# Kernel optimization log

Measured on AMD Instinct MI355X. Metric: run time of the kernel, lower is better.

The kernel has to match this reference:

```python
import jax, jax.numpy as jnp
import numpy as np

ALPHA = 0.2        # LeakyReLU negative slope (config['alpha'])
NEG_INF = -9e15    # mask value from the original code


def setup_inputs() -> dict:
    key = jax.random.key(0)
    k1, k2, k3, k4 = jax.random.split(key, 4)
    N, Fin, Fout = 8192, 512, 256
    inp = jax.random.normal(k1, (N, Fin), dtype=jnp.float32)
    adj = jax.random.randint(k2, (N, N), 0, 2, dtype=jnp.int32)
    # xavier_uniform with gain=1.414
    limW = 1.414 * np.sqrt(6.0 / (Fin + Fout))
    W = jax.random.uniform(k3, (Fin, Fout), dtype=jnp.float32, minval=-limW, maxval=limW)
    lima = 1.414 * np.sqrt(6.0 / (2 * Fout + 1))
    a = jax.random.uniform(k4, (2 * Fout, 1), dtype=jnp.float32, minval=-lima, maxval=lima)
    return {"input": inp, "adj": adj, "W": W, "a": a}


def reference(input, adj, W, a):
    # h: [N, F]
    h = input @ W
    Fout = W.shape[1]
    # The original builds a_input[i, j] = concat(h_i, h_j) and dots with a.
    # Equivalently: e_ij = leakyrelu(h_i . a[:F] + h_j . a[F:]), computed
    # without the O(N^2 * 2F) intermediate.
    s1 = h @ a[:Fout, 0]   # [N] contribution from node i
    s2 = h @ a[Fout:, 0]   # [N] contribution from node j
    e = s1[:, None] + s2[None, :]                     # [N, N]
    e = jnp.where(e > 0, e, ALPHA * e)                # LeakyReLU
    scores = jnp.where(adj > 0, e, NEG_INF)
    attention = jax.nn.softmax(scores, axis=1)        # row-wise softmax
    # dropout is identity in inference mode (training=False)
    h_prime = attention @ h                           # [N, F]
    return jax.nn.elu(h_prime)                        # concat=True path
```

## Files before the change

kernel.cpp:

```cpp
#include <hip/hip_runtime.h>
#include <stdint.h>
#include <stddef.h>


#define N_NODES 8192
#define FIN     512
#define FOUT    256
#define LRALPHA 0.2f
#define MI_SHIFT 16.0f

typedef float f32x4 __attribute__((ext_vector_type(4)));
typedef short s16x8 __attribute__((ext_vector_type(8)));
typedef unsigned short u16x4 __attribute__((ext_vector_type(4)));
typedef int   i32x4 __attribute__((ext_vector_type(4)));

__device__ __forceinline__ short f2bf_rne(float f) {
  uint32_t u = __builtin_bit_cast(uint32_t, f);
  u += 0x7fffu + ((u >> 16) & 1u);
  return (short)(u >> 16);
}
__device__ __forceinline__ short f2bf_fast(float f) {
  uint32_t u = __builtin_bit_cast(uint32_t, f);
  return (short)((u + 0x8000u) >> 16);
}
__device__ __forceinline__ float bf2f(short s) {
  uint32_t u = ((uint32_t)(uint16_t)s) << 16;
  return __builtin_bit_cast(float, u);
}

__global__ __launch_bounds__(256) void k_prep(const float* __restrict__ W,
                                              uint16_t* __restrict__ WThi,
                                              uint16_t* __restrict__ WTlo) {
  const int idx = blockIdx.x * 256 + threadIdx.x;
  const int n = idx >> 9;
  const int k = idx & 511;
  float v = W[k * FOUT + n];
  short h = f2bf_rne(v);
  WThi[idx] = (uint16_t)h;
  WTlo[idx] = (uint16_t)f2bf_rne(v - bf2f(h));
}

__global__ __launch_bounds__(256) void k_gemm_fused(const float* __restrict__ X,
                                                    const uint16_t* __restrict__ WThi,
                                                    const uint16_t* __restrict__ WTlo,
                                                    const float* __restrict__ a,
                                                    uint16_t* __restrict__ HT,
                                                    float* __restrict__ s1g,
                                                    float* __restrict__ s2g) {
  __shared__ float ls1[16], ls2[16];
  __shared__ uint16_t tile[FOUT * 16];
  const int lane = threadIdx.x & 63;
  const int w    = threadIdx.x >> 6;
  const int m    = lane & 15;
  const int quad = lane >> 4;
  const int i0   = blockIdx.x * 16;
  const int colg = w * 64;

  f32x4 acc[4];
#pragma unroll
  for (int cb = 0; cb < 4; ++cb) { f32x4 z = {0.f,0.f,0.f,0.f}; acc[cb] = z; }

  for (int kt = 0; kt < FIN / 32; ++kt) {
    const int k0 = kt * 32 + quad * 8;
    const float* ap = X + (size_t)(i0 + m) * FIN + k0;
    f32x4 a0 = *(const f32x4*)ap;
    f32x4 a1 = *(const f32x4*)(ap + 4);
    s16x8 ahi, alo;
#pragma unroll
    for (int e = 0; e < 4; ++e) {
      short h0 = f2bf_rne(a0[e]); ahi[e] = h0; alo[e] = f2bf_rne(a0[e] - bf2f(h0));
      short h1 = f2bf_rne(a1[e]); ahi[4+e] = h1; alo[4+e] = f2bf_rne(a1[e] - bf2f(h1));
    }
#pragma unroll
    for (int cb = 0; cb < 4; ++cb) {
      const int n = colg + cb * 16 + m;
      s16x8 bhi = *(const s16x8*)(WThi + (size_t)n * FIN + k0);
      s16x8 blo = *(const s16x8*)(WTlo + (size_t)n * FIN + k0);
      acc[cb] = __builtin_amdgcn_mfma_f32_16x16x32_bf16(ahi, bhi, acc[cb], 0, 0, 0);
      acc[cb] = __builtin_amdgcn_mfma_f32_16x16x32_bf16(ahi, blo, acc[cb], 0, 0, 0);
      acc[cb] = __builtin_amdgcn_mfma_f32_16x16x32_bf16(alo, bhi, acc[cb], 0, 0, 0);
    }
  }

  float p1[4] = {0.f,0.f,0.f,0.f}, p2[4] = {0.f,0.f,0.f,0.f};
#pragma unroll
  for (int cb = 0; cb < 4; ++cb) {
    const int n = colg + cb * 16 + m;
    const float a1c = a[n];
    const float a2c = a[FOUT + n];
#pragma unroll
    for (int reg = 0; reg < 4; ++reg) {
      p1[reg] += acc[cb][reg] * a1c;
      p2[reg] += acc[cb][reg] * a2c;
    }
  }
#pragma unroll
  for (int off = 1; off <= 8; off <<= 1)
#pragma unroll
    for (int reg = 0; reg < 4; ++reg) {
      p1[reg] += __shfl_xor(p1[reg], off);
      p2[reg] += __shfl_xor(p2[reg], off);
    }
  if (threadIdx.x < 16) { ls1[threadIdx.x] = 0.f; ls2[threadIdx.x] = 0.f; }
  __syncthreads();
  if (m == 0) {
#pragma unroll
    for (int reg = 0; reg < 4; ++reg) {
      atomicAdd(&ls1[quad * 4 + reg], p1[reg]);
      atomicAdd(&ls2[quad * 4 + reg], p2[reg]);
    }
  }
#pragma unroll
  for (int cb = 0; cb < 4; ++cb) {
    const int col = colg + cb * 16 + m;
    u16x4 pk;
#pragma unroll
    for (int reg = 0; reg < 4; ++reg) pk[reg] = (uint16_t)f2bf_rne(acc[cb][reg]);
    *(u16x4*)(tile + col * 16 + quad * 4) = pk;
  }
  __syncthreads();
  const int t = threadIdx.x;
  if (t < 16) { s1g[i0 + t] = ls1[t]; s2g[i0 + t] = ls2[t]; }
  const uint4* src = (const uint4*)(tile + t * 16);
  uint4 v0 = src[0], v1 = src[1];
  uint4* dst = (uint4*)(HT + (size_t)t * N_NODES + i0);
  dst[0] = v0; dst[1] = v1;
}

__global__ __launch_bounds__(512, 4) void k_attn(const int* __restrict__ adj,
                                                 const uint16_t* __restrict__ HT,
                                                 const float* __restrict__ s1,
                                                 const float* __restrict__ s2,
                                                 float* __restrict__ pout,
                                                 float* __restrict__ pden,
                                                 int split) {
  extern __shared__ char smem[];
  uint16_t* Pl     = (uint16_t*)smem;
  float*    ldsden = (float*)(smem + 16384);
  float*    ls2    = (float*)(smem + 17408);

  const int tid  = threadIdx.x;
  const int lane = tid & 63;
  const int w    = tid >> 6;
  const int m    = lane & 15;
  const int q    = lane >> 4;
  const int i0   = blockIdx.x * 32;
  const int sp   = blockIdx.y;
  const int jrange = N_NODES / split;
  const int jbeg   = sp * jrange;
  const int nphase = jrange / 128;
  const int colg = w * 32;
  const int rtp  = q >> 1;
  const int jq   = (q & 1) * 8;
  const int prow = i0 + rtp * 16 + m;

  for (int o = tid * 4; o < jrange; o += 2048)
    *(f32x4*)(ls2 + o) = *(const f32x4*)(s2 + jbeg + o);

  const float s1r = s1[prow];
  float mi = s1r + MI_SHIFT; mi = mi > 0.f ? mi : LRALPHA * mi;

  f32x4 acc[2][2];
#pragma unroll
  for (int rt = 0; rt < 2; ++rt)
#pragma unroll
    for (int cb = 0; cb < 2; ++cb) { f32x4 z = {0.f,0.f,0.f,0.f}; acc[rt][cb] = z; }
  float den = 0.f;

  const int* arow = adj + (size_t)prow * N_NODES + jbeg + w * 16 + jq;
  const int  pwoff = ((w * 2 + (q & 1)) * 32 + rtp * 16 + m) * 8;

  i32x4 A0 = *(const i32x4*)arow;
  i32x4 A1 = *(const i32x4*)(arow + 4);
  __syncthreads();

#pragma unroll 1
  for (int p = 0; p < nphase; ++p) {
    const int jo = jbeg + p * 128;
    s16x8 B[4][2];
#pragma unroll
    for (int js = 0; js < 4; ++js)
#pragma unroll
      for (int cb = 0; cb < 2; ++cb)
        B[js][cb] = *(const s16x8*)(HT + (size_t)(colg + cb * 16 + m) * N_NODES
                                    + jo + js * 32 + q * 8);
    const int poff = ((p + 1 < nphase) ? (p + 1) : 0) * 128;
    i32x4 nA0 = *(const i32x4*)(arow + poff);
    i32x4 nA1 = *(const i32x4*)(arow + poff + 4);
    f32x4 sv0 = *(const f32x4*)(ls2 + p * 128 + w * 16 + jq);
    f32x4 sv1 = *(const f32x4*)(ls2 + p * 128 + w * 16 + jq + 4);
    s16x8 ap;
#pragma unroll
    for (int e = 0; e < 4; ++e) {
      float x = s1r + sv0[e];
      float t = x > 0.f ? x : LRALPHA * x;
      float pv = __expf(t - mi);
      pv = (A0[e] != 0) ? pv : 0.f;
      den += pv;
      ap[e] = f2bf_fast(pv);
    }
#pragma unroll
    for (int e = 0; e < 4; ++e) {
      float x = s1r + sv1[e];
      float t = x > 0.f ? x : LRALPHA * x;
      float pv = __expf(t - mi);
      pv = (A1[e] != 0) ? pv : 0.f;
      den += pv;
      ap[4 + e] = f2bf_fast(pv);
    }
    uint16_t* Pw = Pl + (p & 1) * 4096;
    *(s16x8*)(Pw + pwoff) = ap;
    __syncthreads();
#pragma unroll
    for (int js = 0; js < 4; ++js) {
      const uint16_t* pc = Pw + ((js * 4 + q) * 32 + m) * 8;
      s16x8 f0 = *(const s16x8*)pc;
      s16x8 f1 = *(const s16x8*)(pc + 128);
      acc[0][0] = __builtin_amdgcn_mfma_f32_16x16x32_bf16(f0, B[js][0], acc[0][0], 0, 0, 0);
      acc[0][1] = __builtin_amdgcn_mfma_f32_16x16x32_bf16(f0, B[js][1], acc[0][1], 0, 0, 0);
      acc[1][0] = __builtin_amdgcn_mfma_f32_16x16x32_bf16(f1, B[js][0], acc[1][0], 0, 0, 0);
      acc[1][1] = __builtin_amdgcn_mfma_f32_16x16x32_bf16(f1, B[js][1], acc[1][1], 0, 0, 0);
    }
    A0 = nA0; A1 = nA1;
  }

  den += __shfl_xor(den, 16);
  if ((q & 1) == 0) ldsden[w * 32 + rtp * 16 + m] = den;
  __syncthreads();
  if (tid < 32) {
    float d = 0.f;
#pragma unroll
    for (int wv = 0; wv < 8; ++wv) d += ldsden[wv * 32 + tid];
    pden[(size_t)sp * N_NODES + i0 + tid] = d;
  }
#pragma unroll
  for (int rt = 0; rt < 2; ++rt)
#pragma unroll
    for (int cb = 0; cb < 2; ++cb)
#pragma unroll
      for (int reg = 0; reg < 4; ++reg) {
        const int row = i0 + rt * 16 + q * 4 + reg;
        const int col = colg + cb * 16 + m;
        pout[((size_t)sp * N_NODES + row) * FOUT + col] = acc[rt][cb][reg];
      }
}

__global__ __launch_bounds__(256) void k_reduce(const float* __restrict__ pout,
                                                const float* __restrict__ pden,
                                                float* __restrict__ out,
                                                int split) {
  const int gid = blockIdx.x * 256 + threadIdx.x;
  const int i = gid >> 6;
  const int c = (gid & 63) << 2;
  f32x4 sum = {0.f,0.f,0.f,0.f};
  float den = 0.f;
  for (int s = 0; s < split; ++s) {
    sum += *(const f32x4*)(pout + ((size_t)s * N_NODES + i) * FOUT + c);
    den += pden[(size_t)s * N_NODES + i];
  }
  const float inv = 1.0f / den;
  f32x4 r;
#pragma unroll
  for (int e = 0; e < 4; ++e) {
    float v = sum[e] * inv;
    r[e] = v > 0.f ? v : (__expf(v) - 1.0f);
  }
  *(f32x4*)(out + (size_t)i * FOUT + c) = r;
}

extern "C" void kernel_launch(void* const* d_in, const int* in_sizes, int n_in,
                              void* d_out, int out_size, void* d_ws, size_t ws_size,
                              hipStream_t stream) {
  const float* X   = (const float*)d_in[0];
  const int*   adj = (const int*)d_in[1];
  const float* W   = (const float*)d_in[2];
  const float* a   = (const float*)d_in[3];
  float* out = (float*)d_out;

  char* ws = (char*)d_ws;
  uint16_t* HT   = (uint16_t*)ws;
  uint16_t* WThi = (uint16_t*)(ws + (4u << 20));
  uint16_t* WTlo = WThi + (size_t)FOUT * FIN;
  float*    s1   = (float*)(ws + (4u << 20) + (512u << 10));
  float*    s2   = s1 + N_NODES;
  float*    pden = s2 + N_NODES;
  const size_t pout_off = (size_t)5u << 20;
  const size_t slab = (size_t)N_NODES * FOUT * sizeof(float);

  int split = (ws_size >= pout_off + 2 * slab) ? 2 : 1;
  float* pout = (split == 1) ? out : (float*)(ws + pout_off);
  const size_t ldsbytes = 17408 + (size_t)(N_NODES / split) * sizeof(float);

  k_prep<<<dim3(512), dim3(256), 0, stream>>>(W, WThi, WTlo);
  k_gemm_fused<<<dim3(N_NODES / 16), dim3(256), 0, stream>>>(X, WThi, WTlo, a, HT, s1, s2);
  k_attn<<<dim3(N_NODES / 32, split), dim3(512), ldsbytes, stream>>>(adj, HT, s1, s2, pout, pden, split);
  k_reduce<<<dim3(N_NODES * FOUT / 4 / 256), dim3(256), 0, stream>>>(pout, pden, out, split);
}
```

Baseline: 503.6 us.

## Store H in MFMA-fragment order, drop LDS s2 staging, raise occupancy and split

The GEMM epilogue now writes H in a fragment-tiled layout, so each lane in the attention kernel loads its B operand as one contiguous 16-byte chunk per MFMA instead of doing strided column reads from a transposed H. B loads move inside the MFMA loop after the barrier. The s2 vector is no longer staged in LDS and is read straight from global memory, which shrinks shared memory to a fixed static size and allows launch bounds of 8 blocks per CU. Split-K over j can now be 4 when the workspace is large enough, which adds more partial-output traffic for the reduce kernel.

```diff
diff --git a/kernel.cpp b/kernel.cpp
--- a/kernel.cpp
+++ b/kernel.cpp
@@ -44,7 +44,7 @@
                                                     const uint16_t* __restrict__ WThi,
                                                     const uint16_t* __restrict__ WTlo,
                                                     const float* __restrict__ a,
-                                                    uint16_t* __restrict__ HT,
+                                                    uint16_t* __restrict__ HTf,
                                                     float* __restrict__ s1g,
                                                     float* __restrict__ s2g) {
   __shared__ float ls1[16], ls2[16];
@@ -121,23 +121,26 @@
   __syncthreads();
   const int t = threadIdx.x;
   if (t < 16) { s1g[i0 + t] = ls1[t]; s2g[i0 + t] = ls2[t]; }
-  const uint4* src = (const uint4*)(tile + t * 16);
-  uint4 v0 = src[0], v1 = src[1];
-  uint4* dst = (uint4*)(HT + (size_t)t * N_NODES + i0);
-  dst[0] = v0; dst[1] = v1;
-}
-
-__global__ __launch_bounds__(512, 4) void k_attn(const int* __restrict__ adj,
-                                                 const uint16_t* __restrict__ HT,
+  const int jt = i0 >> 5;
+  const int qh = (i0 >> 4) & 1;
+  const int c  = t >> 4;
+  const int mm = t & 15;
+#pragma unroll
+  for (int qq = 0; qq < 2; ++qq) {
+    uint4 v = *(const uint4*)(tile + (c * 16 + mm) * 16 + qq * 8);
+    *(uint4*)(HTf + ((((size_t)jt * 16 + c) * 64) + (qh * 2 + qq) * 16 + mm) * 8) = v;
+  }
+}
+
+__global__ __launch_bounds__(512, 8) void k_attn(const int* __restrict__ adj,
+                                                 const uint16_t* __restrict__ HTf,
                                                  const float* __restrict__ s1,
                                                  const float* __restrict__ s2,
                                                  float* __restrict__ pout,
                                                  float* __restrict__ pden,
                                                  int split) {
-  extern __shared__ char smem[];
-  uint16_t* Pl     = (uint16_t*)smem;
-  float*    ldsden = (float*)(smem + 16384);
-  float*    ls2    = (float*)(smem + 17408);
+  __shared__ uint16_t Pl[2][4096];
+  __shared__ float ldsden[256];
 
   const int tid  = threadIdx.x;
   const int lane = tid & 63;
@@ -149,14 +152,10 @@
   const int jrange = N_NODES / split;
   const int jbeg   = sp * jrange;
   const int nphase = jrange / 128;
-  const int colg = w * 32;
   const int rtp  = q >> 1;
   const int jq   = (q & 1) * 8;
   const int prow = i0 + rtp * 16 + m;
 
-  for (int o = tid * 4; o < jrange; o += 2048)
-    *(f32x4*)(ls2 + o) = *(const f32x4*)(s2 + jbeg + o);
-
   const float s1r = s1[prow];
   float mi = s1r + MI_SHIFT; mi = mi > 0.f ? mi : LRALPHA * mi;
 
@@ -168,27 +167,20 @@
   float den = 0.f;
 
   const int* arow = adj + (size_t)prow * N_NODES + jbeg + w * 16 + jq;
+  const float* s2w = s2 + jbeg + w * 16 + jq;
   const int  pwoff = ((w * 2 + (q & 1)) * 32 + rtp * 16 + m) * 8;
+  const uint16_t* hbase = HTf + ((size_t)(jbeg >> 5) * 16 + w * 2) * 64 * 8 + lane * 8;
 
   i32x4 A0 = *(const i32x4*)arow;
   i32x4 A1 = *(const i32x4*)(arow + 4);
-  __syncthreads();
 
 #pragma unroll 1
   for (int p = 0; p < nphase; ++p) {
-    const int jo = jbeg + p * 128;
-    s16x8 B[4][2];
-#pragma unroll
-    for (int js = 0; js < 4; ++js)
-#pragma unroll
-      for (int cb = 0; cb < 2; ++cb)
-        B[js][cb] = *(const s16x8*)(HT + (size_t)(colg + cb * 16 + m) * N_NODES
-                                    + jo + js * 32 + q * 8);
     const int poff = ((p + 1 < nphase) ? (p + 1) : 0) * 128;
     i32x4 nA0 = *(const i32x4*)(arow + poff);
     i32x4 nA1 = *(const i32x4*)(arow + poff + 4);
-    f32x4 sv0 = *(const f32x4*)(ls2 + p * 128 + w * 16 + jq);
-    f32x4 sv1 = *(const f32x4*)(ls2 + p * 128 + w * 16 + jq + 4);
+    f32x4 sv0 = *(const f32x4*)(s2w + p * 128);
+    f32x4 sv1 = *(const f32x4*)(s2w + p * 128 + 4);
     s16x8 ap;
 #pragma unroll
     for (int e = 0; e < 4; ++e) {
@@ -208,20 +200,23 @@
       den += pv;
       ap[4 + e] = f2bf_fast(pv);
     }
-    uint16_t* Pw = Pl + (p & 1) * 4096;
+    uint16_t* Pw = Pl[p & 1];
     *(s16x8*)(Pw + pwoff) = ap;
+    A0 = nA0; A1 = nA1;
     __syncthreads();
+    const uint16_t* hp = hbase + ((size_t)p * 4) * (16 * 64 * 8);
 #pragma unroll
     for (int js = 0; js < 4; ++js) {
+      s16x8 b0 = *(const s16x8*)(hp + (size_t)js * (16 * 64 * 8));
+      s16x8 b1 = *(const s16x8*)(hp + (size_t)js * (16 * 64 * 8) + 64 * 8);
       const uint16_t* pc = Pw + ((js * 4 + q) * 32 + m) * 8;
       s16x8 f0 = *(const s16x8*)pc;
       s16x8 f1 = *(const s16x8*)(pc + 128);
-      acc[0][0] = __builtin_amdgcn_mfma_f32_16x16x32_bf16(f0, B[js][0], acc[0][0], 0, 0, 0);
-      acc[0][1] = __builtin_amdgcn_mfma_f32_16x16x32_bf16(f0, B[js][1], acc[0][1], 0, 0, 0);
-      acc[1][0] = __builtin_amdgcn_mfma_f32_16x16x32_bf16(f1, B[js][0], acc[1][0], 0, 0, 0);
-      acc[1][1] = __builtin_amdgcn_mfma_f32_16x16x32_bf16(f1, B[js][1], acc[1][1], 0, 0, 0);
-    }
-    A0 = nA0; A1 = nA1;
+      acc[0][0] = __builtin_amdgcn_mfma_f32_16x16x32_bf16(f0, b0, acc[0][0], 0, 0, 0);
+      acc[0][1] = __builtin_amdgcn_mfma_f32_16x16x32_bf16(f0, b1, acc[0][1], 0, 0, 0);
+      acc[1][0] = __builtin_amdgcn_mfma_f32_16x16x32_bf16(f1, b0, acc[1][0], 0, 0, 0);
+      acc[1][1] = __builtin_amdgcn_mfma_f32_16x16x32_bf16(f1, b1, acc[1][1], 0, 0, 0);
+    }
   }
 
   den += __shfl_xor(den, 16);
@@ -233,6 +228,7 @@
     for (int wv = 0; wv < 8; ++wv) d += ldsden[wv * 32 + tid];
     pden[(size_t)sp * N_NODES + i0 + tid] = d;
   }
+  const int colg = w * 32;
 #pragma unroll
   for (int rt = 0; rt < 2; ++rt)
 #pragma unroll
@@ -278,7 +274,7 @@
   float* out = (float*)d_out;
 
   char* ws = (char*)d_ws;
-  uint16_t* HT   = (uint16_t*)ws;
+  uint16_t* HTf  = (uint16_t*)ws;
   uint16_t* WThi = (uint16_t*)(ws + (4u << 20));
   uint16_t* WTlo = WThi + (size_t)FOUT * FIN;
   float*    s1   = (float*)(ws + (4u << 20) + (512u << 10));
@@ -287,12 +283,14 @@
   const size_t pout_off = (size_t)5u << 20;
   const size_t slab = (size_t)N_NODES * FOUT * sizeof(float);
 
-  int split = (ws_size >= pout_off + 2 * slab) ? 2 : 1;
+  int split;
+  if      (ws_size >= pout_off + 4 * slab) split = 4;
+  else if (ws_size >= pout_off + 2 * slab) split = 2;
+  else                                     split = 1;
   float* pout = (split == 1) ? out : (float*)(ws + pout_off);
-  const size_t ldsbytes = 17408 + (size_t)(N_NODES / split) * sizeof(float);
 
   k_prep<<<dim3(512), dim3(256), 0, stream>>>(W, WThi, WTlo);
-  k_gemm_fused<<<dim3(N_NODES / 16), dim3(256), 0, stream>>>(X, WThi, WTlo, a, HT, s1, s2);
-  k_attn<<<dim3(N_NODES / 32, split), dim3(512), ldsbytes, stream>>>(adj, HT, s1, s2, pout, pden, split);
+  k_gemm_fused<<<dim3(N_NODES / 16), dim3(256), 0, stream>>>(X, WThi, WTlo, a, HTf, s1, s2);
+  k_attn<<<dim3(N_NODES / 32, split), dim3(512), 0, stream>>>(adj, HTf, s1, s2, pout, pden, split);
   k_reduce<<<dim3(N_NODES * FOUT / 4 / 256), dim3(256), 0, stream>>>(pout, pden, out, split);
 }
```

Measured after the change: 474.0 us. 1.06x faster.
